# Performance work log

Hardware: AMD Instinct MI355X
Metric: run time of the kernel (lower is better)

Reference implementation:

```python
import jax, jax.numpy as jnp
from jax import lax
import numpy as np
import math

D_MODEL = 1024
D_STATE = 16
D_CONV = 4
EXPAND = 2
D_INNER = EXPAND * D_MODEL  # 2048
DT_RANK = math.ceil(D_MODEL / 16)  # 64
BATCH = 2
SEQ = 2048


def setup_inputs() -> dict:
    key = jax.random.key(0)
    ks = jax.random.split(key, 8)
    s = 0.02
    x = jax.random.normal(ks[0], (BATCH, SEQ, D_MODEL), jnp.float32)
    ln_w = jnp.ones((D_MODEL,), jnp.float32)
    ln_b = jnp.zeros((D_MODEL,), jnp.float32)
    in_proj_w = jax.random.normal(ks[1], (D_MODEL, 2 * D_INNER), jnp.float32) * s
    conv_w = jax.random.normal(ks[2], (D_INNER, D_CONV), jnp.float32) * s
    conv_b = jnp.zeros((D_INNER,), jnp.float32)
    x_proj_w = jax.random.normal(ks[3], (D_INNER, DT_RANK + 2 * D_STATE), jnp.float32) * s
    dt_proj_w = jax.random.normal(ks[4], (DT_RANK, D_INNER), jnp.float32) * (DT_RANK ** -0.5)
    # mamba-ssm dt bias init: softplus^{-1}(dt) with dt ~ logUniform(1e-3, 1e-1)
    dt = jnp.exp(jax.random.uniform(ks[5], (D_INNER,), jnp.float32)
                 * (jnp.log(0.1) - jnp.log(0.001)) + jnp.log(0.001))
    dt_proj_b = dt + jnp.log(-jnp.expm1(-dt))
    # S4D-real init: A = -[1..d_state] per channel
    A_log = jnp.log(jnp.broadcast_to(
        jnp.arange(1, D_STATE + 1, dtype=jnp.float32), (D_INNER, D_STATE)))
    D_skip = jnp.ones((D_INNER,), jnp.float32)
    out_proj_w = jax.random.normal(ks[6], (D_INNER, D_MODEL), jnp.float32) * s
    return dict(x=x, ln_w=ln_w, ln_b=ln_b, in_proj_w=in_proj_w, conv_w=conv_w,
                conv_b=conv_b, x_proj_w=x_proj_w, dt_proj_w=dt_proj_w,
                dt_proj_b=dt_proj_b, A_log=A_log, D_skip=D_skip,
                out_proj_w=out_proj_w)


def _layernorm(x, w, b):
    mu = x.mean(-1, keepdims=True)
    var = ((x - mu) ** 2).mean(-1, keepdims=True)
    return (x - mu) * lax.rsqrt(var + 1e-5) * w + b


def _mamba(xn, in_proj_w, conv_w, conv_b, x_proj_w, dt_proj_w, dt_proj_b,
           A_log, D_skip, out_proj_w):
    # in_proj -> split into conv path and gate z
    xz = xn @ in_proj_w                      # [B, L, 2*d_inner]
    xi, z = jnp.split(xz, 2, axis=-1)
    # causal depthwise conv1d over time
    xc = jnp.pad(xi.transpose(0, 2, 1), ((0, 0), (0, 0), (D_CONV - 1, 0)))
    xc = lax.conv_general_dilated(xc, conv_w[:, None, :], (1,), 'VALID',
                                  feature_group_count=D_INNER,
                                  dimension_numbers=('NCH', 'OIH', 'NCH'))
    xc = jax.nn.silu(xc.transpose(0, 2, 1) + conv_b)   # [B, L, d_inner]
    # input-dependent dt, B, C
    dbc = xc @ x_proj_w                      # [B, L, dt_rank + 2*d_state]
    dt = jax.nn.softplus(dbc[..., :DT_RANK] @ dt_proj_w + dt_proj_b)
    Bm = dbc[..., DT_RANK:DT_RANK + D_STATE]  # [B, L, d_state]
    Cm = dbc[..., DT_RANK + D_STATE:]         # [B, L, d_state]
    A = -jnp.exp(A_log)                       # [d_inner, d_state]

    def step(h, inp):
        u_t, dt_t, b_t, c_t = inp             # [B,d_inner],[B,d_inner],[B,S],[B,S]
        h = jnp.exp(dt_t[..., None] * A) * h + (dt_t * u_t)[..., None] * b_t[:, None, :]
        y = jnp.einsum('bds,bs->bd', h, c_t)
        return h, y

    h0 = jnp.zeros((xn.shape[0], D_INNER, D_STATE), xn.dtype)
    _, ys = lax.scan(step, h0, (xc.transpose(1, 0, 2), dt.transpose(1, 0, 2),
                                Bm.transpose(1, 0, 2), Cm.transpose(1, 0, 2)))
    y = ys.transpose(1, 0, 2) + xc * D_skip
    y = y * jax.nn.silu(z)
    return y @ out_proj_w


def reference(x, ln_w, ln_b, in_proj_w, conv_w, conv_b, x_proj_w, dt_proj_w,
              dt_proj_b, A_log, D_skip, out_proj_w):
    xn = _layernorm(x, ln_w, ln_b)
    return x + _mamba(xn, in_proj_w, conv_w, conv_b, x_proj_w, dt_proj_w,
                      dt_proj_b, A_log, D_skip, out_proj_w)
```

## Files before the change

### kernel.cpp

```cpp
#include <hip/hip_runtime.h>
#include <math.h>

#define NROWS 4096
#define DM    1024
#define DI    2048
#define DTR   64
#define DST   16
#define NCHUNK 16
#define CHLEN  128
#define XKS   8
#define XKL   256

typedef __attribute__((ext_vector_type(8))) short bf16x8;
typedef __attribute__((ext_vector_type(4))) float f32x4;

__device__ __forceinline__ unsigned short f2bf(float f) {
  unsigned u = __float_as_uint(f);
  u = (u + 0x7fffu + ((u >> 16) & 1u)) >> 16;
  return (unsigned short)u;
}
__device__ __forceinline__ float softplus_f(float v) {
  return fmaxf(v, 0.f) + log1pf(__expf(-fabsf(v)));
}
__device__ __forceinline__ float silu_f(float v) {
  return v * (1.f / (1.f + __expf(-v)));
}
__device__ __forceinline__ void gload_lds16(const void* g, void* l) {
  __builtin_amdgcn_global_load_lds(
      (const __attribute__((address_space(1))) void*)g,
      (__attribute__((address_space(3))) void*)l, 16, 0, 0);
}

__global__ __launch_bounds__(256) void ln_kernel(const float* __restrict__ x,
                                                 const float* __restrict__ w,
                                                 const float* __restrict__ b,
                                                 unsigned short* __restrict__ xnb) {
  const int row = blockIdx.x;
  const int tid = threadIdx.x;
  const float4 v = ((const float4*)(x + (size_t)row * DM))[tid];
  float s  = v.x + v.y + v.z + v.w;
  float ss = v.x * v.x + v.y * v.y + v.z * v.z + v.w * v.w;
  for (int off = 32; off > 0; off >>= 1) {
    s  += __shfl_down(s, off);
    ss += __shfl_down(ss, off);
  }
  __shared__ float red[4][2];
  if ((tid & 63) == 0) { red[tid >> 6][0] = s; red[tid >> 6][1] = ss; }
  __syncthreads();
  const float fs  = red[0][0] + red[1][0] + red[2][0] + red[3][0];
  const float fss = red[0][1] + red[1][1] + red[2][1] + red[3][1];
  const float mu  = fs * (1.f / DM);
  const float var = fss * (1.f / DM) - mu * mu;
  const float rs  = rsqrtf(var + 1e-5f);
  const float4 wv = ((const float4*)w)[tid];
  const float4 bv = ((const float4*)b)[tid];
  ushort4 o;
  o.x = f2bf((v.x - mu) * rs * wv.x + bv.x);
  o.y = f2bf((v.y - mu) * rs * wv.y + bv.y);
  o.z = f2bf((v.z - mu) * rs * wv.z + bv.z);
  o.w = f2bf((v.w - mu) * rs * wv.w + bv.w);
  ((ushort4*)(xnb + (size_t)row * DM))[tid] = o;
}

__global__ __launch_bounds__(256) void transpose_bf16(const float* __restrict__ W,
                                                      unsigned short* __restrict__ Wt,
                                                      int K, int N) {
  __shared__ float t[32][33];
  const int n0 = blockIdx.x * 32, k0 = blockIdx.y * 32;
  const int tx = threadIdx.x & 31, ty = threadIdx.x >> 5;
#pragma unroll
  for (int i = 0; i < 4; i++)
    t[ty + i * 8][tx] = W[(size_t)(k0 + ty + i * 8) * N + n0 + tx];
  __syncthreads();
#pragma unroll
  for (int i = 0; i < 4; i++)
    Wt[(size_t)(n0 + ty + i * 8) * K + k0 + tx] = f2bf(t[tx][ty + i * 8]);
}

template <int EPI>
__global__ __launch_bounds__(256) void gemm_mfma(
    const unsigned short* __restrict__ A, const unsigned short* __restrict__ Bt,
    float* __restrict__ C, int M, int N, int K, const float* __restrict__ resid) {
  __shared__ unsigned short Asl[128 * 32];
  __shared__ unsigned short Bsl[128 * 32];
  const int tid  = threadIdx.x;
  const int wave = tid >> 6, lane = tid & 63;
  const int wr = wave >> 1, wc = wave & 1;
  const int m0 = blockIdx.y * 128, n0 = blockIdx.x * 128;
  const int srow = lane >> 2;
  const int skoff = (lane & 3) * 8;
  f32x4 acc[4][4] = {};
  for (int k0 = 0; k0 < K; k0 += 32) {
    __syncthreads();
#pragma unroll
    for (int i = 0; i < 2; i++) {
      const int c = wave * 2 + i;
      gload_lds16(A  + (size_t)(m0 + c * 16 + srow) * K + k0 + skoff, &Asl[c * 512]);
      gload_lds16(Bt + (size_t)(n0 + c * 16 + srow) * K + k0 + skoff, &Bsl[c * 512]);
    }
    __syncthreads();
    bf16x8 af[4], bfr[4];
#pragma unroll
    for (int m = 0; m < 4; m++)
      af[m] = *(const bf16x8*)&Asl[(wr * 64 + m * 16 + (lane & 15)) * 32 + (lane >> 4) * 8];
#pragma unroll
    for (int n = 0; n < 4; n++)
      bfr[n] = *(const bf16x8*)&Bsl[(wc * 64 + n * 16 + (lane & 15)) * 32 + (lane >> 4) * 8];
#pragma unroll
    for (int m = 0; m < 4; m++)
#pragma unroll
      for (int n = 0; n < 4; n++)
        acc[m][n] = __builtin_amdgcn_mfma_f32_16x16x32_bf16(af[m], bfr[n], acc[m][n], 0, 0, 0);
  }
#pragma unroll
  for (int m = 0; m < 4; m++) {
#pragma unroll
    for (int n = 0; n < 4; n++) {
      const int col = n0 + wc * 64 + n * 16 + (lane & 15);
#pragma unroll
      for (int r = 0; r < 4; r++) {
        const int row = m0 + wr * 64 + m * 16 + (lane >> 4) * 4 + r;
        float v = acc[m][n][r];
        if (EPI == 2) v += resid[(size_t)row * N + col];
        C[(size_t)row * N + col] = v;
      }
    }
  }
}

__global__ __launch_bounds__(256) void xproj_splitk(
    const float* __restrict__ A,
    const float* __restrict__ B,
    float* __restrict__ part) {
  __shared__ float AsT[32][68];
  __shared__ float Bs[32][96];
  const int ks = blockIdx.x;
  const int r0 = blockIdx.y * 64;
  const int tid = threadIdx.x;
  const int rg = tid >> 4;
  const int cg = tid & 15;
  const int arow = tid >> 2;
  const int ac   = (tid & 3) * 2;
  const int bk   = tid >> 3;
  const int bc   = tid & 7;
  float acc[4][6] = {};
  const int k0base = ks * XKL;
  for (int kt = 0; kt < XKL; kt += 32) {
    const int k0 = k0base + kt;
    const float4 a0 = *(const float4*)&A[(size_t)(r0 + arow) * DI + k0 + ac * 4];
    const float4 a1 = *(const float4*)&A[(size_t)(r0 + arow) * DI + k0 + (ac + 1) * 4];
    const float4 b0 = *(const float4*)&B[(size_t)(k0 + bk) * 96 + bc * 4];
    const float4 b1 = *(const float4*)&B[(size_t)(k0 + bk) * 96 + (bc + 8) * 4];
    const float4 b2 = *(const float4*)&B[(size_t)(k0 + bk) * 96 + (bc + 16) * 4];
    __syncthreads();
#pragma unroll
    for (int j = 0; j < 4; j++) AsT[ac * 4 + j][arow] = (&a0.x)[j];
#pragma unroll
    for (int j = 0; j < 4; j++) AsT[(ac + 1) * 4 + j][arow] = (&a1.x)[j];
    *(float4*)&Bs[bk][bc * 4] = b0;
    *(float4*)&Bs[bk][(bc + 8) * 4] = b1;
    *(float4*)&Bs[bk][(bc + 16) * 4] = b2;
    __syncthreads();
#pragma unroll
    for (int k = 0; k < 32; k++) {
      const float4 av = *(const float4*)&AsT[k][rg * 4];
      const float2 bv0 = *(const float2*)&Bs[k][cg * 6];
      const float2 bv1 = *(const float2*)&Bs[k][cg * 6 + 2];
      const float2 bv2 = *(const float2*)&Bs[k][cg * 6 + 4];
#pragma unroll
      for (int i = 0; i < 4; i++) {
        const float a = (&av.x)[i];
        acc[i][0] += a * bv0.x; acc[i][1] += a * bv0.y;
        acc[i][2] += a * bv1.x; acc[i][3] += a * bv1.y;
        acc[i][4] += a * bv2.x; acc[i][5] += a * bv2.y;
      }
    }
  }
#pragma unroll
  for (int i = 0; i < 4; i++) {
    const int row = r0 + rg * 4 + i;
    float* p = &part[((size_t)ks * NROWS + row) * 96 + cg * 6];
#pragma unroll
    for (int j = 0; j < 3; j++)
      *(float2*)&p[j * 2] = make_float2(acc[i][j * 2], acc[i][j * 2 + 1]);
  }
}

__global__ __launch_bounds__(256) void xproj_reduce(const float* __restrict__ part,
                                                    float* __restrict__ dbc) {
  const int i = blockIdx.x * 256 + threadIdx.x;
  float s = 0.f;
#pragma unroll
  for (int ks = 0; ks < XKS; ks++) s += part[(size_t)ks * (NROWS * 96) + i];
  dbc[i] = s;
}

template <int EPI>
__global__ __launch_bounds__(256) void gemm_kernel(
    const float* __restrict__ A, const float* __restrict__ B,
    float* __restrict__ C, int M, int N, int K, int lda, int ldb, int ldc,
    const float* __restrict__ bias) {
  __shared__ float As[64][20];
  __shared__ float Bs[16][64];
  const int tid = threadIdx.x;
  const int m0 = blockIdx.y * 64, n0 = blockIdx.x * 64;
  const int tx = tid & 15, ty = tid >> 4;
  const int am = tid >> 2, ak4 = (tid & 3) << 2;
  const int bk = tid >> 4, bn4 = (tid & 15) << 2;
  const bool bin = (n0 + bn4) < N;
  float acc[4][4] = {};
  for (int k0 = 0; k0 < K; k0 += 16) {
    const float4 av = *(const float4*)&A[(size_t)(m0 + am) * lda + k0 + ak4];
    float4 bv = make_float4(0.f, 0.f, 0.f, 0.f);
    if (bin) bv = *(const float4*)&B[(size_t)(k0 + bk) * ldb + n0 + bn4];
    __syncthreads();
    *(float4*)&As[am][ak4] = av;
    *(float4*)&Bs[bk][bn4] = bv;
    __syncthreads();
#pragma unroll
    for (int k4 = 0; k4 < 4; k4++) {
      float4 aa[4], bb[4];
#pragma unroll
      for (int i = 0; i < 4; i++) aa[i] = *(const float4*)&As[ty * 4 + i][k4 * 4];
#pragma unroll
      for (int kk = 0; kk < 4; kk++) bb[kk] = *(const float4*)&Bs[k4 * 4 + kk][tx * 4];
#pragma unroll
      for (int kk = 0; kk < 4; kk++) {
#pragma unroll
        for (int i = 0; i < 4; i++) {
          const float a = (&aa[i].x)[kk];
          acc[i][0] += a * bb[kk].x;
          acc[i][1] += a * bb[kk].y;
          acc[i][2] += a * bb[kk].z;
          acc[i][3] += a * bb[kk].w;
        }
      }
    }
  }
#pragma unroll
  for (int i = 0; i < 4; i++) {
    const int row = m0 + ty * 4 + i;
    const int col = n0 + tx * 4;
    if (col < N) {
      float4 o = make_float4(acc[i][0], acc[i][1], acc[i][2], acc[i][3]);
      if (EPI == 1) {
        const float4 bi = *(const float4*)&bias[col];
        o.x = softplus_f(o.x + bi.x);
        o.y = softplus_f(o.y + bi.y);
        o.z = softplus_f(o.z + bi.z);
        o.w = softplus_f(o.w + bi.w);
      }
      *(float4*)&C[(size_t)row * ldc + col] = o;
    }
  }
}

__global__ __launch_bounds__(256) void conv_silu_kernel(const float* __restrict__ xz,
                                                        const float* __restrict__ cw,
                                                        const float* __restrict__ cb,
                                                        float* __restrict__ xc) {
  const int idx = blockIdx.x * 256 + threadIdx.x;
  const int d4 = (idx & 511) << 2;
  const int r = idx >> 9;
  const int t = r & 2047;
  const float4 w0 = *(const float4*)&cw[(d4 + 0) * 4];
  const float4 w1 = *(const float4*)&cw[(d4 + 1) * 4];
  const float4 w2 = *(const float4*)&cw[(d4 + 2) * 4];
  const float4 w3 = *(const float4*)&cw[(d4 + 3) * 4];
  float4 acc = *(const float4*)&cb[d4];
#pragma unroll
  for (int j = 0; j < 4; j++) {
    const int tj = t - 3 + j;
    if (tj >= 0) {
      const float4 xv = *(const float4*)&xz[(size_t)(r - 3 + j) * 4096 + d4];
      acc.x += xv.x * (&w0.x)[j];
      acc.y += xv.y * (&w1.x)[j];
      acc.z += xv.z * (&w2.x)[j];
      acc.w += xv.w * (&w3.x)[j];
    }
  }
  acc.x = silu_f(acc.x); acc.y = silu_f(acc.y);
  acc.z = silu_f(acc.z); acc.w = silu_f(acc.w);
  *(float4*)&xc[(size_t)r * DI + d4] = acc;
}

__global__ __launch_bounds__(256) void scan_pass1(
    const float* __restrict__ dt, const float* __restrict__ xc,
    const float* __restrict__ dbc, const float* __restrict__ A_log,
    float* __restrict__ aprod_buf, float* __restrict__ hout_buf) {
  const int b  = blockIdx.x >> 11;
  const int dg = (blockIdx.x >> 4) & 127;
  const int c  = blockIdx.x & 15;
  const int d0 = dg * 16;
  const int tid = threadIdx.x;
  const int g = tid >> 4, s = tid & 15;
  const float A = -expf(A_log[(d0 + g) * DST + s]);
  float h = 0.f, ap = 1.f;
  __shared__ float sdt[64][16], su[64][16], sB[64][16];
  const int base_r = b * 2048 + c * CHLEN;
  for (int t0 = 0; t0 < CHLEN; t0 += 64) {
    __syncthreads();
#pragma unroll
    for (int i = 0; i < 4; i++) {
      const int flat = tid + i * 256;
      const int tt = flat >> 4, dd = flat & 15;
      const size_t r = base_r + t0 + tt;
      sdt[tt][dd] = dt[r * 4096 + d0 + dd];
      su[tt][dd]  = xc[r * 2048 + d0 + dd];
      sB[tt][dd]  = dbc[r * 96 + DTR + dd];
    }
    __syncthreads();
#pragma unroll 8
    for (int tt = 0; tt < 64; tt++) {
      const float dtv = sdt[tt][g];
      const float a = __expf(dtv * A);
      h = a * h + (dtv * su[tt][g]) * sB[tt][s];
      ap *= a;
    }
  }
  const int idx = ((b * 128 + dg) * NCHUNK + c) * 256 + tid;
  aprod_buf[idx] = ap;
  hout_buf[idx]  = h;
}

__global__ __launch_bounds__(256) void scan_fixup(const float* __restrict__ aprod_buf,
                                                  float* __restrict__ hout_buf) {
  const int t = blockIdx.x * 256 + threadIdx.x;
  const int seq = t >> 8;
  const int lane = t & 255;
  const int base = seq * NCHUNK * 256 + lane;
  float h = 0.f;
#pragma unroll
  for (int c = 0; c < NCHUNK; c++) {
    const float a = aprod_buf[base + c * 256];
    const float o = hout_buf[base + c * 256];
    hout_buf[base + c * 256] = h;
    h = a * h + o;
  }
}

__global__ __launch_bounds__(256) void scan_pass2(
    const float* __restrict__ dt, const float* __restrict__ xc,
    const float* __restrict__ dbc, const float* __restrict__ A_log,
    const float* __restrict__ Dskip, const float* __restrict__ z,
    const float* __restrict__ hin_buf, unsigned short* __restrict__ y16) {
  const int b  = blockIdx.x >> 11;
  const int dg = (blockIdx.x >> 4) & 127;
  const int c  = blockIdx.x & 15;
  const int d0 = dg * 16;
  const int tid = threadIdx.x;
  const int g = tid >> 4, s = tid & 15;
  const float A = -expf(A_log[(d0 + g) * DST + s]);
  float h = hin_buf[((b * 128 + dg) * NCHUNK + c) * 256 + tid];
  __shared__ float sdt[64][16], su[64][16], sB[64][16], sC[64][16], sy[64][16];
  const int base_r = b * 2048 + c * CHLEN;
  for (int t0 = 0; t0 < CHLEN; t0 += 64) {
    __syncthreads();
#pragma unroll
    for (int i = 0; i < 4; i++) {
      const int flat = tid + i * 256;
      const int tt = flat >> 4, dd = flat & 15;
      const size_t r = base_r + t0 + tt;
      sdt[tt][dd] = dt[r * 4096 + d0 + dd];
      su[tt][dd]  = xc[r * 2048 + d0 + dd];
      sB[tt][dd]  = dbc[r * 96 + DTR + dd];
      sC[tt][dd]  = dbc[r * 96 + DTR + DST + dd];
    }
    __syncthreads();
#pragma unroll 4
    for (int tt = 0; tt < 64; tt++) {
      const float dtv = sdt[tt][g];
      const float a = __expf(dtv * A);
      h = a * h + (dtv * su[tt][g]) * sB[tt][s];
      float p = h * sC[tt][s];
      p += __shfl_xor(p, 8);
      p += __shfl_xor(p, 4);
      p += __shfl_xor(p, 2);
      p += __shfl_xor(p, 1);
      if (s == 0) sy[tt][g] = p;
    }
    __syncthreads();
#pragma unroll
    for (int i = 0; i < 4; i++) {
      const int flat = tid + i * 256;
      const int tt = flat >> 4, dd = flat & 15;
      const size_t r = base_r + t0 + tt;
      float yv = sy[tt][dd] + su[tt][dd] * Dskip[d0 + dd];
      const float zv = z[r * 4096 + d0 + dd];
      yv *= silu_f(zv);
      y16[r * 2048 + d0 + dd] = f2bf(yv);
    }
  }
}

extern "C" void kernel_launch(void* const* d_in, const int* in_sizes, int n_in,
                              void* d_out, int out_size, void* d_ws, size_t ws_size,
                              hipStream_t stream) {
  const float* x         = (const float*)d_in[0];
  const float* ln_w      = (const float*)d_in[1];
  const float* ln_b      = (const float*)d_in[2];
  const float* in_proj_w = (const float*)d_in[3];
  const float* conv_w    = (const float*)d_in[4];
  const float* conv_b    = (const float*)d_in[5];
  const float* x_proj_w  = (const float*)d_in[6];
  const float* dt_proj_w = (const float*)d_in[7];
  const float* dt_proj_b = (const float*)d_in[8];
  const float* A_log     = (const float*)d_in[9];
  const float* D_skip    = (const float*)d_in[10];
  const float* out_proj_w= (const float*)d_in[11];
  float* out = (float*)d_out;
  float* ws  = (float*)d_ws;

  unsigned short* xnb  = (unsigned short*)ws;
  float* part  = ws;
  float* aprod = ws + (2u << 20);
  float* hout  = ws + (3u << 20);
  float* xz    = ws + (4u << 20);
  float* xc    = ws + (20u << 20);
  float* dbc   = ws + (28u << 20);
  unsigned short* wtin  = (unsigned short*)(ws + (29u << 20));
  unsigned short* wtout = (unsigned short*)(ws + (31u << 20));
  unsigned short* yb16  = (unsigned short*)(ws + (32u << 20));
  float* dtb = xz;
  float* zp  = xz + DI;

  transpose_bf16<<<dim3(4096 / 32, 1024 / 32), 256, 0, stream>>>(in_proj_w, wtin, DM, 4096);
  transpose_bf16<<<dim3(1024 / 32, 2048 / 32), 256, 0, stream>>>(out_proj_w, wtout, DI, DM);
  ln_kernel<<<NROWS, 256, 0, stream>>>(x, ln_w, ln_b, xnb);
  gemm_mfma<0><<<dim3(32, 32), 256, 0, stream>>>(xnb, wtin, xz, NROWS, 4096, DM, nullptr);
  conv_silu_kernel<<<8192, 256, 0, stream>>>(xz, conv_w, conv_b, xc);
  xproj_splitk<<<dim3(XKS, 64), 256, 0, stream>>>(xc, x_proj_w, part);
  xproj_reduce<<<(NROWS * 96) / 256, 256, 0, stream>>>(part, dbc);
  gemm_kernel<1><<<dim3(32, 64), 256, 0, stream>>>(dbc, dt_proj_w, dtb,
      NROWS, DI, DTR, 96, DI, 4096, dt_proj_b);
  scan_pass1<<<4096, 256, 0, stream>>>(dtb, xc, dbc, A_log, aprod, hout);
  scan_fixup<<<256, 256, 0, stream>>>(aprod, hout);
  scan_pass2<<<4096, 256, 0, stream>>>(dtb, xc, dbc, A_log, D_skip, zp, hout, yb16);
  gemm_mfma<2><<<dim3(8, 32), 256, 0, stream>>>(yb16, wtout, out, NROWS, DM, DI, x);
}
```

Baseline: 472.0 us.

## Restructure selective scan to one thread per channel with register-resident states

The chunked scan now gives each thread one inner channel and keeps all 16 state values in registers. This removes the LDS staging, the block barriers and the per-step cross-lane shuffle reduction for y, and global loads become coalesced along the channel dimension. The chunk count doubles to 32 chunks of 64 steps to recover parallelism, and the carry buffers are re-laid out by state and channel to match. The trade-off is far fewer threads in flight (512 blocks instead of 4096), so the scan may become latency-bound from low occupancy.

```diff
diff --git a/kernel.cpp b/kernel.cpp
--- a/kernel.cpp
+++ b/kernel.cpp
@@ -6,8 +6,8 @@
 #define DI    2048
 #define DTR   64
 #define DST   16
-#define NCHUNK 16
-#define CHLEN  128
+#define NCHUNK 32
+#define CHLEN  64
 #define XKS   8
 #define XKL   256
 
@@ -285,56 +285,55 @@
 }
 
 __global__ __launch_bounds__(256) void scan_pass1(
-    const float* __restrict__ dt, const float* __restrict__ xc,
-    const float* __restrict__ dbc, const float* __restrict__ A_log,
+    const float* __restrict__ dt,
+    const float* __restrict__ xc,
+    const float* __restrict__ dbc,
+    const float* __restrict__ A_log,
     float* __restrict__ aprod_buf, float* __restrict__ hout_buf) {
-  const int b  = blockIdx.x >> 11;
-  const int dg = (blockIdx.x >> 4) & 127;
-  const int c  = blockIdx.x & 15;
-  const int d0 = dg * 16;
-  const int tid = threadIdx.x;
-  const int g = tid >> 4, s = tid & 15;
-  const float A = -expf(A_log[(d0 + g) * DST + s]);
-  float h = 0.f, ap = 1.f;
-  __shared__ float sdt[64][16], su[64][16], sB[64][16];
+  const int bx = blockIdx.x;
+  const int b = bx >> 8, c = (bx >> 3) & 31, dblk = bx & 7;
+  const int d = dblk * 256 + threadIdx.x;
+  float A[DST], h[DST], ap[DST];
+#pragma unroll
+  for (int s = 0; s < DST; s++) {
+    A[s] = -expf(A_log[d * DST + s]);
+    h[s] = 0.f; ap[s] = 1.f;
+  }
   const int base_r = b * 2048 + c * CHLEN;
-  for (int t0 = 0; t0 < CHLEN; t0 += 64) {
-    __syncthreads();
-#pragma unroll
-    for (int i = 0; i < 4; i++) {
-      const int flat = tid + i * 256;
-      const int tt = flat >> 4, dd = flat & 15;
-      const size_t r = base_r + t0 + tt;
-      sdt[tt][dd] = dt[r * 4096 + d0 + dd];
-      su[tt][dd]  = xc[r * 2048 + d0 + dd];
-      sB[tt][dd]  = dbc[r * 96 + DTR + dd];
-    }
-    __syncthreads();
-#pragma unroll 8
-    for (int tt = 0; tt < 64; tt++) {
-      const float dtv = sdt[tt][g];
-      const float a = __expf(dtv * A);
-      h = a * h + (dtv * su[tt][g]) * sB[tt][s];
-      ap *= a;
-    }
-  }
-  const int idx = ((b * 128 + dg) * NCHUNK + c) * 256 + tid;
-  aprod_buf[idx] = ap;
-  hout_buf[idx]  = h;
+#pragma unroll 2
+  for (int t = 0; t < CHLEN; t++) {
+    const size_t r = base_r + t;
+    const float dtv = dt[r * 4096 + d];
+    const float uv  = xc[r * 2048 + d];
+    const float du = dtv * uv;
+    const float* bc = &dbc[r * 96 + DTR];
+#pragma unroll
+    for (int s = 0; s < DST; s++) {
+      const float a = __expf(dtv * A[s]);
+      h[s] = a * h[s] + du * bc[s];
+      ap[s] *= a;
+    }
+  }
+  const size_t base = ((size_t)(b * NCHUNK + c) * DST) * DI + d;
+#pragma unroll
+  for (int s = 0; s < DST; s++) {
+    aprod_buf[base + (size_t)s * DI] = ap[s];
+    hout_buf[base + (size_t)s * DI]  = h[s];
+  }
 }
 
 __global__ __launch_bounds__(256) void scan_fixup(const float* __restrict__ aprod_buf,
                                                   float* __restrict__ hout_buf) {
-  const int t = blockIdx.x * 256 + threadIdx.x;
-  const int seq = t >> 8;
-  const int lane = t & 255;
-  const int base = seq * NCHUNK * 256 + lane;
+  const int gl = blockIdx.x * 256 + threadIdx.x;
+  const int d = gl & 2047, s = (gl >> 11) & 15, b = gl >> 15;
+  const size_t base = ((size_t)(b * NCHUNK) * DST + s) * DI + d;
+  const size_t stride = (size_t)DST * DI;
   float h = 0.f;
 #pragma unroll
   for (int c = 0; c < NCHUNK; c++) {
-    const float a = aprod_buf[base + c * 256];
-    const float o = hout_buf[base + c * 256];
-    hout_buf[base + c * 256] = h;
+    const float a = aprod_buf[base + c * stride];
+    const float o = hout_buf[base + c * stride];
+    hout_buf[base + c * stride] = h;
     h = a * h + o;
   }
 }
@@ -344,52 +343,35 @@
     const float* __restrict__ dbc, const float* __restrict__ A_log,
     const float* __restrict__ Dskip, const float* __restrict__ z,
     const float* __restrict__ hin_buf, unsigned short* __restrict__ y16) {
-  const int b  = blockIdx.x >> 11;
-  const int dg = (blockIdx.x >> 4) & 127;
-  const int c  = blockIdx.x & 15;
-  const int d0 = dg * 16;
-  const int tid = threadIdx.x;
-  const int g = tid >> 4, s = tid & 15;
-  const float A = -expf(A_log[(d0 + g) * DST + s]);
-  float h = hin_buf[((b * 128 + dg) * NCHUNK + c) * 256 + tid];
-  __shared__ float sdt[64][16], su[64][16], sB[64][16], sC[64][16], sy[64][16];
+  const int bx = blockIdx.x;
+  const int b = bx >> 8, c = (bx >> 3) & 31, dblk = bx & 7;
+  const int d = dblk * 256 + threadIdx.x;
+  float A[DST], h[DST];
+  const size_t base = ((size_t)(b * NCHUNK + c) * DST) * DI + d;
+#pragma unroll
+  for (int s = 0; s < DST; s++) {
+    A[s] = -expf(A_log[d * DST + s]);
+    h[s] = hin_buf[base + (size_t)s * DI];
+  }
+  const float dsk = Dskip[d];
   const int base_r = b * 2048 + c * CHLEN;
-  for (int t0 = 0; t0 < CHLEN; t0 += 64) {
-    __syncthreads();
-#pragma unroll
-    for (int i = 0; i < 4; i++) {
-      const int flat = tid + i * 256;
-      const int tt = flat >> 4, dd = flat & 15;
-      const size_t r = base_r + t0 + tt;
-      sdt[tt][dd] = dt[r * 4096 + d0 + dd];
-      su[tt][dd]  = xc[r * 2048 + d0 + dd];
-      sB[tt][dd]  = dbc[r * 96 + DTR + dd];
-      sC[tt][dd]  = dbc[r * 96 + DTR + DST + dd];
-    }
-    __syncthreads();
-#pragma unroll 4
-    for (int tt = 0; tt < 64; tt++) {
-      const float dtv = sdt[tt][g];
-      const float a = __expf(dtv * A);
-      h = a * h + (dtv * su[tt][g]) * sB[tt][s];
-      float p = h * sC[tt][s];
-      p += __shfl_xor(p, 8);
-      p += __shfl_xor(p, 4);
-      p += __shfl_xor(p, 2);
-      p += __shfl_xor(p, 1);
-      if (s == 0) sy[tt][g] = p;
-    }
-    __syncthreads();
-#pragma unroll
-    for (int i = 0; i < 4; i++) {
-      const int flat = tid + i * 256;
-      const int tt = flat >> 4, dd = flat & 15;
-      const size_t r = base_r + t0 + tt;
-      float yv = sy[tt][dd] + su[tt][dd] * Dskip[d0 + dd];
-      const float zv = z[r * 4096 + d0 + dd];
-      yv *= silu_f(zv);
-      y16[r * 2048 + d0 + dd] = f2bf(yv);
-    }
+#pragma unroll 2
+  for (int t = 0; t < CHLEN; t++) {
+    const size_t r = base_r + t;
+    const float dtv = dt[r * 4096 + d];
+    const float uv  = xc[r * 2048 + d];
+    const float zv  = z[r * 4096 + d];
+    const float du = dtv * uv;
+    const float* bc = &dbc[r * 96 + DTR];
+    float y = 0.f;
+#pragma unroll
+    for (int s = 0; s < DST; s++) {
+      const float a = __expf(dtv * A[s]);
+      h[s] = a * h[s] + du * bc[s];
+      y += h[s] * bc[DST + s];
+    }
+    y = (y + uv * dsk) * silu_f(zv);
+    y16[r * 2048 + d] = f2bf(y);
   }
 }
 
@@ -413,8 +395,8 @@
 
   unsigned short* xnb  = (unsigned short*)ws;
   float* part  = ws;
-  float* aprod = ws + (2u << 20);
-  float* hout  = ws + (3u << 20);
+  float* aprod = ws;
+  float* hout  = ws + (2u << 20);
   float* xz    = ws + (4u << 20);
   float* xc    = ws + (20u << 20);
   float* dbc   = ws + (28u << 20);
@@ -433,8 +415,8 @@
   xproj_reduce<<<(NROWS * 96) / 256, 256, 0, stream>>>(part, dbc);
   gemm_kernel<1><<<dim3(32, 64), 256, 0, stream>>>(dbc, dt_proj_w, dtb,
       NROWS, DI, DTR, 96, DI, 4096, dt_proj_b);
-  scan_pass1<<<4096, 256, 0, stream>>>(dtb, xc, dbc, A_log, aprod, hout);
+  scan_pass1<<<2 * NCHUNK * 8, 256, 0, stream>>>(dtb, xc, dbc, A_log, aprod, hout);
   scan_fixup<<<256, 256, 0, stream>>>(aprod, hout);
-  scan_pass2<<<4096, 256, 0, stream>>>(dtb, xc, dbc, A_log, D_skip, zp, hout, yb16);
+  scan_pass2<<<2 * NCHUNK * 8, 256, 0, stream>>>(dtb, xc, dbc, A_log, D_skip, zp, hout, yb16);
   gemm_mfma<2><<<dim3(8, 32), 256, 0, stream>>>(yb16, wtout, out, NROWS, DM, DI, x);
 }
```

After: 408.1 us. 1.16x faster.
